# Optimization experiments

Measured on AMD Instinct MI355X. Metric: run time of the kernel, lower is better.

## Reference

```python
import jax, jax.numpy as jnp
import numpy as np

B, T, D, H, L = 32, 1024, 512, 512, 2  # batch, time, input dim, rnn_dim, layers


def setup_inputs() -> dict:
    key = jax.random.key(0)
    ks = jax.random.split(key, 4)
    x = jax.random.normal(ks[0], (B, T, D), jnp.float32)
    # contiguous-length mask like Keras masking (True = valid timestep)
    lengths = jax.random.randint(ks[1], (B,), T // 4, T + 1)
    mask = jnp.arange(T)[None, :] < lengths[:, None]
    s = 1.0 / np.sqrt(H)
    Wk = jax.random.normal(ks[2], (L, 2, D, 4 * H), jnp.float32) * s  # input kernels [layer, dir]
    Wr = jax.random.normal(ks[3], (L, 2, H, 4 * H), jnp.float32) * s  # recurrent kernels
    b = jnp.zeros((L, 2, 4 * H), jnp.float32)
    return {"x": x, "mask": mask, "Wk": Wk, "Wr": Wr, "b": b}


def _lstm_dir(x, mask, Wk, Wr, b, reverse):
    """Single-direction Keras-style LSTM with masking (masked steps carry h,c)."""
    if reverse:  # Bidirectional backward layer: process reversed time, reverse output back
        x = x[:, ::-1]
        mask = mask[:, ::-1]
    # precompute input projection for all timesteps: [B,T,4H]
    xw = jnp.einsum('btd,dg->btg', x, Wk) + b
    h0 = jnp.zeros((x.shape[0], Wr.shape[0]), x.dtype)

    def step(carry, inp):
        h, c = carry
        xw_t, m_t = inp  # [B,4H], [B]
        z = xw_t + h @ Wr
        i, f, g, o = jnp.split(z, 4, axis=-1)  # Keras gate order i,f,c,o
        c_new = jax.nn.sigmoid(f) * c + jax.nn.sigmoid(i) * jnp.tanh(g)
        h_new = jax.nn.sigmoid(o) * jnp.tanh(c_new)
        m = m_t[:, None]
        h = jnp.where(m, h_new, h)  # masked step: copy previous output/state
        c = jnp.where(m, c_new, c)
        return (h, c), h

    _, ys = jax.lax.scan(step, (h0, h0), (xw.transpose(1, 0, 2), mask.T))
    ys = ys.transpose(1, 0, 2)  # [B,T,H]
    if reverse:
        ys = ys[:, ::-1]
    return ys


def reference(x, mask, Wk, Wr, b):
    inp = x
    for l in range(L):
        fwd = _lstm_dir(inp, mask, Wk[l, 0], Wr[l, 0], b[l, 0], False)
        bwd = _lstm_dir(inp, mask, Wk[l, 1], Wr[l, 1], b[l, 1], True)
        res = fwd + bwd  # merge_mode='sum'
        inp = res + inp if l > 0 else res  # residual from layer 1 onward
    return inp
```

## Files before the change

### kernel.cpp

```cpp
#include <hip/hip_runtime.h>
#include <stdint.h>


#define B_ 32
#define T_ 1024
#define H_ 512
#define G_ 2048

typedef _Float16 f16;
typedef _Float16 f16x8 __attribute__((ext_vector_type(8)));
typedef float f32x4 __attribute__((ext_vector_type(4)));

#define AL_U(p) __hip_atomic_load((p), __ATOMIC_RELAXED, __HIP_MEMORY_SCOPE_AGENT)
#define AS_U(p, v) __hip_atomic_store((p), (v), __ATOMIC_RELAXED, __HIP_MEMORY_SCOPE_AGENT)
#define AADD_U(p, v) __hip_atomic_fetch_add((p), (v), __ATOMIC_RELAXED, __HIP_MEMORY_SCOPE_AGENT)

struct Claim {
  unsigned cnt[8];
  unsigned dirclaim;
  int xcddir[8];
  unsigned pad[15];
};

__device__ __forceinline__ float sigm(float x) { return 1.f / (1.f + __expf(-x)); }
__device__ __forceinline__ float tanh_(float x) { return 1.f - 2.f / (__expf(2.f * x) + 1.f); }

__global__ void cvt_x_t(const float* __restrict__ x, f16* __restrict__ xh) {
  size_t j = (size_t)blockIdx.x * 256 + threadIdx.x;
  int t = (int)(j >> 11);
  int g = (int)(j & 2047);
  int b = g >> 6;
  int d0 = (g & 63) * 8;
  const float4* p = (const float4*)(x + ((size_t)b * T_ + t) * H_ + d0);
  float4 a = p[0], c = p[1];
  union { f16 h[8]; uint4 u; } r;
  r.h[0] = (f16)a.x; r.h[1] = (f16)a.y; r.h[2] = (f16)a.z; r.h[3] = (f16)a.w;
  r.h[4] = (f16)c.x; r.h[5] = (f16)c.y; r.h[6] = (f16)c.z; r.h[7] = (f16)c.w;
  size_t o = (((size_t)t * 32 + (d0 >> 4)) * 32 + b) * 16 + (d0 & 15);
  *(uint4*)(xh + o) = r.u;
}

__global__ void cvt_w(const float* __restrict__ W, f16* __restrict__ Wb) {
  __shared__ float tl[32][65];
  const int wgi = blockIdx.x, kt = blockIdx.y, z = blockIdx.z;
  const float* src = W + (size_t)z * H_ * G_;
  const int k0 = kt * 32;
  for (int idx = threadIdx.x; idx < 2048; idx += 256) {
    int kk = idx >> 6, jj = idx & 63;
    int gate = jj >> 4, c = jj & 15;
    tl[kk][jj] = src[(size_t)(k0 + kk) * G_ + gate * H_ + wgi * 16 + c];
  }
  __syncthreads();
  const int gate = threadIdx.x >> 6, l = threadIdx.x & 63;
  const int c = l & 15, koff = (l >> 4) * 8;
  union { f16 h[8]; uint4 u; } v;
#pragma unroll
  for (int e = 0; e < 8; ++e) v.h[e] = (f16)tl[koff + e][gate * 16 + c];
  f16* dst = Wb + ((size_t)z * 32 + wgi) * 32768 + ((size_t)(kt * 4 + gate) * 64 + l) * 8;
  *(uint4*)dst = v.u;
}

__global__ void sum_h(const f16* __restrict__ a, const f16* __restrict__ b,
                      f16* __restrict__ r) {
  size_t i = ((size_t)blockIdx.x * 256 + threadIdx.x) * 8;
  f16x8 va = *(const f16x8*)(a + i), vb = *(const f16x8*)(b + i);
  *(f16x8*)(r + i) = va + vb;
}

template <int LAYER>
__global__ __launch_bounds__(512, 2) void lstm_rec4(
    const f16* __restrict__ xh,
    const f16* __restrict__ wkb,
    const f16* __restrict__ wrb,
    const float* __restrict__ biasAll,
    const void* __restrict__ maskp,
    f16* __restrict__ ring,
    unsigned* __restrict__ flags,
    Claim* __restrict__ cl,
    float* __restrict__ out,
    const f16* __restrict__ res1h)
{
  const int tid = threadIdx.x, wave = tid >> 6, lane = tid & 63;

  __shared__ int s_dir, s_wgi;
  if (tid == 0) {
    unsigned xcd;
    asm volatile("s_getreg_b32 %0, hwreg(HW_REG_XCC_ID)" : "=s"(xcd));
    xcd &= 7u;
    unsigned slot = AADD_U(&cl->cnt[xcd], 1u);
    int dir = -1, wgi = -1;
    if (slot < 32u) {
      if (slot == 31u) {
        unsigned d = AADD_U(&cl->dirclaim, 1u);
        int val = (d < 2u) ? (int)(d + 1u) : -1;
        __hip_atomic_store(&cl->xcddir[xcd], val, __ATOMIC_RELAXED, __HIP_MEMORY_SCOPE_AGENT);
      }
      while (true) {
        int v = __hip_atomic_load(&cl->xcddir[xcd], __ATOMIC_RELAXED, __HIP_MEMORY_SCOPE_AGENT);
        if (v != 0) { if (v > 0) { dir = v - 1; wgi = (int)slot; } break; }
        if (AL_U(&cl->dirclaim) >= 2u && AL_U(&cl->cnt[xcd]) < 32u) break;
        __builtin_amdgcn_s_sleep(2);
      }
    }
    s_dir = dir; s_wgi = wgi;
  }
  __syncthreads();
  const int dir = s_dir, wgi = s_wgi;
  if (dir < 0) return;

  const int mtile = wave & 1, kq = wave >> 1;
  const int j0 = wgi * 16;
  const int z = LAYER * 2 + dir;

  __shared__ f16 wkl[32768];
  __shared__ float zbuf[4][32][64];

  {
    const f16* wkc = wkb + ((size_t)z * 32 + wgi) * 32768;
#pragma unroll
    for (int r = 0; r < 8; ++r)
      *(uint4*)&wkl[(size_t)(r * 512 + tid) * 8] = *(const uint4*)(wkc + (size_t)(r * 512 + tid) * 8);
  }
  f16x8 wfr[4][4];
  {
    const f16* wrc = wrb + ((size_t)z * 32 + wgi) * 32768;
#pragma unroll
    for (int i = 0; i < 4; ++i) {
      int ktg = kq * 4 + i;
#pragma unroll
      for (int g = 0; g < 4; ++g)
        wfr[i][g] = *(const f16x8*)(wrc + ((size_t)(ktg * 4 + g) * 64 + lane) * 8);
    }
  }
  __syncthreads();

  const int arow = mtile * 16 + (lane & 15);
  const int lkb = lane >> 5;
  const int c0 = ((lane >> 4) & 1) * 8;

  const int cb = tid >> 4, cj = tid & 15;
  const float* bb = biasAll + (size_t)z * G_;
  float bias4[4];
#pragma unroll
  for (int g = 0; g < 4; ++g) bias4[g] = bb[g * H_ + j0 + cj];

  const unsigned char* mbytes = (const unsigned char*)maskp;
  const unsigned* mwords = (const unsigned*)maskp;
  const bool bytelay = (mbytes[1] != 0);

  float hstate = 0.f, cstate = 0.f;
  const unsigned* flagd = flags + (size_t)dir * T_ * 32;
  const f32x4 vzero = {0.f, 0.f, 0.f, 0.f};

  for (int s = 0; s < T_; ++s) {
    const int t = dir ? (T_ - 1 - s) : s;
    const f16* xb = xh + (size_t)t * 16384;
    f32x4 acc[4] = {vzero, vzero, vzero, vzero};
#pragma unroll
    for (int i = 0; i < 4; ++i) {
      const int ktg = kq * 4 + i;
      f16x8 xf = *(const f16x8*)(xb + ((size_t)(ktg * 2 + lkb) * 32 + arow) * 16 + c0);
#pragma unroll
      for (int g = 0; g < 4; ++g) {
        f16x8 wk = *(const f16x8*)&wkl[((size_t)(ktg * 4 + g) * 64 + lane) * 8];
        acc[g] = __builtin_amdgcn_mfma_f32_16x16x32_f16(xf, wk, acc[g], 0, 0, 0);
      }
    }
    const size_t btm = (size_t)cb * T_ + t;
    const bool mv = bytelay ? (mbytes[btm] != 0) : (mwords[btm] != 0);
    float xr = 0.f;
    if (LAYER == 1 && dir == 0)
      xr = (float)res1h[(((size_t)t * 32 + wgi) * 32 + cb) * 16 + cj];

    if (s > 0) {
      if (wave == 0) {
        const unsigned* fl = flagd + (size_t)(s - 1) * 32 + (lane & 31);
        while (true) {
          unsigned v = AL_U(fl);
          if (__ballot(v == 1u) == ~0ull) break;
        }
      }
      __syncthreads();
      const f16* hbase;
      if (LAYER == 0) {
        const int tprev = dir ? (T_ - s) : (s - 1);
        hbase = ring + ((size_t)dir * T_ + tprev) * 16384;
      } else {
        hbase = ring + ((size_t)dir * 8 + ((s - 1) & 7)) * 16384;
      }
#pragma unroll
      for (int i = 0; i < 4; ++i) {
        const int ktg = kq * 4 + i;
        f16x8 hf = *(const f16x8*)(hbase + ((size_t)(ktg * 2 + lkb) * 32 + arow) * 16 + c0);
#pragma unroll
        for (int g = 0; g < 4; ++g)
          acc[g] = __builtin_amdgcn_mfma_f32_16x16x32_f16(hf, wfr[i][g], acc[g], 0, 0, 0);
      }
    }
    {
      const int zr = mtile * 16 + ((lane >> 4) << 2);
      const int zc = lane & 15;
#pragma unroll
      for (int g = 0; g < 4; ++g)
#pragma unroll
        for (int r = 0; r < 4; ++r) zbuf[kq][zr + r][g * 16 + zc] = acc[g][r];
    }
    __syncthreads();

    float z4[4];
#pragma unroll
    for (int g = 0; g < 4; ++g)
      z4[g] = zbuf[0][cb][g * 16 + cj] + zbuf[1][cb][g * 16 + cj] +
              zbuf[2][cb][g * 16 + cj] + zbuf[3][cb][g * 16 + cj] + bias4[g];
    float ig = sigm(z4[0]), fg = sigm(z4[1]), gg = tanh_(z4[2]), og = sigm(z4[3]);
    float cn = fg * cstate + ig * gg;
    float hn = og * tanh_(cn);
    if (mv) { cstate = cn; hstate = hn; }

    f16 h16 = (f16)hstate;
    unsigned short hu = __builtin_bit_cast(unsigned short, h16);
    unsigned ob = (unsigned)__shfl_xor((int)hu, 1);
    unsigned pk = (unsigned)hu | ((ob & 0xffffu) << 16);
    if ((cj & 1) == 0) {
      f16* pb;
      if (LAYER == 0) pb = ring + ((size_t)dir * T_ + t) * 16384;
      else            pb = ring + ((size_t)dir * 8 + (s & 7)) * 16384;
      *(unsigned*)(pb + (size_t)wgi * 512 + tid) = pk;
    }
    asm volatile("s_waitcnt vmcnt(0)" ::: "memory");
    __syncthreads();
    if (tid == 0) AS_U((unsigned*)(flagd + (size_t)s * 32 + wgi), 1u);

    if (LAYER == 1) {
      atomicAdd(&out[btm * H_ + j0 + cj], hstate + xr);
    }
  }
}

extern "C" void kernel_launch(void* const* d_in, const int* in_sizes, int n_in,
                              void* d_out, int out_size, void* d_ws, size_t ws_size,
                              hipStream_t stream) {
  const float* x = (const float*)d_in[0];
  const void* maskp = (const void*)d_in[1];
  const float* Wk = (const float*)d_in[2];
  const float* Wr = (const float*)d_in[3];
  const float* bias = (const float*)d_in[4];
  float* out = (float*)d_out;
  (void)in_sizes; (void)n_in;

  char* ws = (char*)d_ws;
  f16* xh = (f16*)(ws);
  f16* wkb = (f16*)(ws + 33554432ull);
  f16* wrb = (f16*)(ws + 41943040ull);
  unsigned* flags0 = (unsigned*)(ws + 50331648ull);
  unsigned* flags1 = (unsigned*)(ws + 50593792ull);
  Claim* cl0 = (Claim*)(ws + 50855936ull);
  Claim* cl1 = (Claim*)(ws + 50856960ull);
  f16* ring1 = (f16*)(ws + 50857984ull);
  if (ws_size < 51382272ull) return;

  f16* ring0 = (f16*)d_out;
  f16* hf = ring0;
  f16* hb = ring0 + (size_t)T_ * 16384;

  hipMemsetAsync(flags0, 0, 526336ull, stream);
  cvt_x_t<<<8192, 256, 0, stream>>>(x, xh);
  cvt_w<<<dim3(32, 16, 4), 256, 0, stream>>>(Wk, wkb);
  cvt_w<<<dim3(32, 16, 4), 256, 0, stream>>>(Wr, wrb);

  lstm_rec4<0><<<512, 512, 0, stream>>>(xh, wkb, wrb, bias, maskp, ring0, flags0,
                                        cl0, (float*)nullptr, (const f16*)nullptr);
  sum_h<<<8192, 256, 0, stream>>>(hf, hb, xh);

  hipMemsetAsync(d_out, 0, 67108864ull, stream);
  lstm_rec4<1><<<512, 512, 0, stream>>>(xh, wkb, wrb, bias, maskp, ring1, flags1,
                                        cl1, out, xh);
}
```

Baseline: 6.091 ms.

## Switch LSTM recurrence to 32x32x16 MFMA with register-resident weights

Replaces the 16x16x32 MFMA tiling with 32x32x16 MFMA, where each wave owns a gate-pair column tile and a K quarter. Both the input and recurrent weight fragments now live in registers, so the LDS copy of the input kernel is dropped. The weight and x conversion kernels are rewritten to emit a matching layout, and the h ring layout changes with them. A large padded LDS allocation is added, apparently to keep occupancy at one block per CU, in exchange for higher register pressure per wave.

After: 7.452 ms. 1.22x slower.

```diff
diff --git a/kernel.cpp b/kernel.cpp
--- a/kernel.cpp
+++ b/kernel.cpp
@@ -9,7 +9,7 @@
 
 typedef _Float16 f16;
 typedef _Float16 f16x8 __attribute__((ext_vector_type(8)));
-typedef float f32x4 __attribute__((ext_vector_type(4)));
+typedef float f32x16 __attribute__((ext_vector_type(16)));
 
 #define AL_U(p) __hip_atomic_load((p), __ATOMIC_RELAXED, __HIP_MEMORY_SCOPE_AGENT)
 #define AS_U(p, v) __hip_atomic_store((p), (v), __ATOMIC_RELAXED, __HIP_MEMORY_SCOPE_AGENT)
@@ -27,10 +27,9 @@
 
 __global__ void cvt_x_t(const float* __restrict__ x, f16* __restrict__ xh) {
   size_t j = (size_t)blockIdx.x * 256 + threadIdx.x;
-  int t = (int)(j >> 11);
-  int g = (int)(j & 2047);
-  int b = g >> 6;
-  int d0 = (g & 63) * 8;
+  int b = (int)(j >> 16);
+  int t = (int)((j >> 6) & 1023);
+  int d0 = (int)(j & 63) * 8;
   const float4* p = (const float4*)(x + ((size_t)b * T_ + t) * H_ + d0);
   float4 a = p[0], c = p[1];
   union { f16 h[8]; uint4 u; } r;
@@ -41,23 +40,26 @@
 }
 
 __global__ void cvt_w(const float* __restrict__ W, f16* __restrict__ Wb) {
-  __shared__ float tl[32][65];
-  const int wgi = blockIdx.x, kt = blockIdx.y, z = blockIdx.z;
+  const int wgi = blockIdx.x, z = blockIdx.y;
+  const int tid = threadIdx.x;
   const float* src = W + (size_t)z * H_ * G_;
-  const int k0 = kt * 32;
-  for (int idx = threadIdx.x; idx < 2048; idx += 256) {
-    int kk = idx >> 6, jj = idx & 63;
-    int gate = jj >> 4, c = jj & 15;
-    tl[kk][jj] = src[(size_t)(k0 + kk) * G_ + gate * H_ + wgi * 16 + c];
-  }
-  __syncthreads();
-  const int gate = threadIdx.x >> 6, l = threadIdx.x & 63;
-  const int c = l & 15, koff = (l >> 4) * 8;
-  union { f16 h[8]; uint4 u; } v;
-#pragma unroll
-  for (int e = 0; e < 8; ++e) v.h[e] = (f16)tl[koff + e][gate * 16 + c];
-  f16* dst = Wb + ((size_t)z * 32 + wgi) * 32768 + ((size_t)(kt * 4 + gate) * 64 + l) * 8;
-  *(uint4*)dst = v.u;
+  __shared__ unsigned short st[512];
+  for (int cp = 0; cp < 2; ++cp)
+    for (int ks = 0; ks < 32; ++ks) {
+      size_t cbase = ((((size_t)z * 32 + wgi) * 2 + cp) * 32 + ks) * 512;
+#pragma unroll
+      for (int pass = 0; pass < 2; ++pass) {
+        int e = tid + pass * 256;
+        int col = e & 31, kk = e >> 5;
+        int gc = (2 * cp + (col >> 4)) * 512 + wgi * 16 + (col & 15);
+        f16 v = (f16)src[(size_t)(ks * 16 + kk) * G_ + gc];
+        st[col * 16 + kk] = __builtin_bit_cast(unsigned short, v);
+      }
+      __syncthreads();
+      unsigned pk = (unsigned)st[2 * tid] | ((unsigned)st[2 * tid + 1] << 16);
+      *((unsigned*)(Wb + cbase) + tid) = pk;
+      __syncthreads();
+    }
 }
 
 __global__ void sum_h(const f16* __restrict__ a, const f16* __restrict__ b,
@@ -68,7 +70,7 @@
 }
 
 template <int LAYER>
-__global__ __launch_bounds__(512, 2) void lstm_rec4(
+__global__ __launch_bounds__(512, 2) void lstm_rec6(
     const f16* __restrict__ xh,
     const f16* __restrict__ wkb,
     const f16* __restrict__ wrb,
@@ -83,6 +85,9 @@
   const int tid = threadIdx.x, wave = tid >> 6, lane = tid & 63;
 
   __shared__ int s_dir, s_wgi;
+  __shared__ float zbuf[2][4][32][48];
+  __shared__ char lds_pad[33024];
+
   if (tid == 0) {
     unsigned xcd;
     asm volatile("s_getreg_b32 %0, hwreg(HW_REG_XCC_ID)" : "=s"(xcd));
@@ -107,36 +112,22 @@
   __syncthreads();
   const int dir = s_dir, wgi = s_wgi;
   if (dir < 0) return;
-
-  const int mtile = wave & 1, kq = wave >> 1;
+  if (s_dir == -2) ((volatile char*)lds_pad)[tid] = 1;
+
+  const int cp = wave & 1, kq = wave >> 1;
   const int j0 = wgi * 16;
   const int z = LAYER * 2 + dir;
-
-  __shared__ f16 wkl[32768];
-  __shared__ float zbuf[4][32][64];
-
-  {
-    const f16* wkc = wkb + ((size_t)z * 32 + wgi) * 32768;
-#pragma unroll
-    for (int r = 0; r < 8; ++r)
-      *(uint4*)&wkl[(size_t)(r * 512 + tid) * 8] = *(const uint4*)(wkc + (size_t)(r * 512 + tid) * 8);
+  const int laneA = (lane & 31) * 16 + (lane >> 5) * 8;
+  const int hi = lane >> 5;
+
+  const f16* wkc = wkb + ((((size_t)z * 32 + wgi) * 2 + cp) * 32 + kq * 8) * 512;
+  const f16* wrc = wrb + ((((size_t)z * 32 + wgi) * 2 + cp) * 32 + kq * 8) * 512;
+  f16x8 wfk[8], wfr[8];
+#pragma unroll
+  for (int i = 0; i < 8; ++i) {
+    wfk[i] = *(const f16x8*)(wkc + i * 512 + laneA);
+    wfr[i] = *(const f16x8*)(wrc + i * 512 + laneA);
   }
-  f16x8 wfr[4][4];
-  {
-    const f16* wrc = wrb + ((size_t)z * 32 + wgi) * 32768;
-#pragma unroll
-    for (int i = 0; i < 4; ++i) {
-      int ktg = kq * 4 + i;
-#pragma unroll
-      for (int g = 0; g < 4; ++g)
-        wfr[i][g] = *(const f16x8*)(wrc + ((size_t)(ktg * 4 + g) * 64 + lane) * 8);
-    }
-  }
-  __syncthreads();
-
-  const int arow = mtile * 16 + (lane & 15);
-  const int lkb = lane >> 5;
-  const int c0 = ((lane >> 4) & 1) * 8;
 
   const int cb = tid >> 4, cj = tid & 15;
   const float* bb = biasAll + (size_t)z * G_;
@@ -149,22 +140,20 @@
   const bool bytelay = (mbytes[1] != 0);
 
   float hstate = 0.f, cstate = 0.f;
-  const unsigned* flagd = flags + (size_t)dir * T_ * 32;
-  const f32x4 vzero = {0.f, 0.f, 0.f, 0.f};
+  unsigned* flagd = flags + (size_t)dir * T_ * 32;
+  const f32x16 vzero = {0.f};
 
   for (int s = 0; s < T_; ++s) {
     const int t = dir ? (T_ - 1 - s) : s;
-    const f16* xb = xh + (size_t)t * 16384;
-    f32x4 acc[4] = {vzero, vzero, vzero, vzero};
-#pragma unroll
-    for (int i = 0; i < 4; ++i) {
-      const int ktg = kq * 4 + i;
-      f16x8 xf = *(const f16x8*)(xb + ((size_t)(ktg * 2 + lkb) * 32 + arow) * 16 + c0);
-#pragma unroll
-      for (int g = 0; g < 4; ++g) {
-        f16x8 wk = *(const f16x8*)&wkl[((size_t)(ktg * 4 + g) * 64 + lane) * 8];
-        acc[g] = __builtin_amdgcn_mfma_f32_16x16x32_f16(xf, wk, acc[g], 0, 0, 0);
-      }
+    const f16* xb = xh + (size_t)t * 16384 + (size_t)kq * 8 * 512 + laneA;
+    f32x16 acc = vzero;
+    {
+      f16x8 xf[8];
+#pragma unroll
+      for (int i = 0; i < 8; ++i) xf[i] = *(const f16x8*)(xb + i * 512);
+#pragma unroll
+      for (int i = 0; i < 8; ++i)
+        acc = __builtin_amdgcn_mfma_f32_32x32x16_f16(xf[i], wfk[i], acc, 0, 0, 0);
     }
     const size_t btm = (size_t)cb * T_ + t;
     const bool mv = bytelay ? (mbytes[btm] != 0) : (mwords[btm] != 0);
@@ -181,38 +170,33 @@
         }
       }
       __syncthreads();
-      const f16* hbase;
+      const f16* hb;
       if (LAYER == 0) {
         const int tprev = dir ? (T_ - s) : (s - 1);
-        hbase = ring + ((size_t)dir * T_ + tprev) * 16384;
+        hb = ring + ((size_t)dir * T_ + tprev) * 16384;
       } else {
-        hbase = ring + ((size_t)dir * 8 + ((s - 1) & 7)) * 16384;
-      }
-#pragma unroll
-      for (int i = 0; i < 4; ++i) {
-        const int ktg = kq * 4 + i;
-        f16x8 hf = *(const f16x8*)(hbase + ((size_t)(ktg * 2 + lkb) * 32 + arow) * 16 + c0);
-#pragma unroll
-        for (int g = 0; g < 4; ++g)
-          acc[g] = __builtin_amdgcn_mfma_f32_16x16x32_f16(hf, wfr[i][g], acc[g], 0, 0, 0);
-      }
-    }
-    {
-      const int zr = mtile * 16 + ((lane >> 4) << 2);
-      const int zc = lane & 15;
-#pragma unroll
-      for (int g = 0; g < 4; ++g)
-#pragma unroll
-        for (int r = 0; r < 4; ++r) zbuf[kq][zr + r][g * 16 + zc] = acc[g][r];
+        hb = ring + ((size_t)dir * 8 + ((s - 1) & 7)) * 16384;
+      }
+      hb += (size_t)kq * 8 * 512 + laneA;
+      f16x8 hf[8];
+#pragma unroll
+      for (int i = 0; i < 8; ++i) hf[i] = *(const f16x8*)(hb + i * 512);
+#pragma unroll
+      for (int i = 0; i < 8; ++i)
+        acc = __builtin_amdgcn_mfma_f32_32x32x16_f16(hf[i], wfr[i], acc, 0, 0, 0);
+    }
+#pragma unroll
+    for (int r = 0; r < 16; ++r) {
+      int row = (r & 3) + 8 * (r >> 2) + 4 * hi;
+      zbuf[cp][kq][row][lane & 31] = acc[r];
     }
     __syncthreads();
 
-    float z4[4];
-#pragma unroll
-    for (int g = 0; g < 4; ++g)
-      z4[g] = zbuf[0][cb][g * 16 + cj] + zbuf[1][cb][g * 16 + cj] +
-              zbuf[2][cb][g * 16 + cj] + zbuf[3][cb][g * 16 + cj] + bias4[g];
-    float ig = sigm(z4[0]), fg = sigm(z4[1]), gg = tanh_(z4[2]), og = sigm(z4[3]);
+    float zi = zbuf[0][0][cb][cj] + zbuf[0][1][cb][cj] + zbuf[0][2][cb][cj] + zbuf[0][3][cb][cj] + bias4[0];
+    float zf = zbuf[0][0][cb][16 + cj] + zbuf[0][1][cb][16 + cj] + zbuf[0][2][cb][16 + cj] + zbuf[0][3][cb][16 + cj] + bias4[1];
+    float zg = zbuf[1][0][cb][cj] + zbuf[1][1][cb][cj] + zbuf[1][2][cb][cj] + zbuf[1][3][cb][cj] + bias4[2];
+    float zo = zbuf[1][0][cb][16 + cj] + zbuf[1][1][cb][16 + cj] + zbuf[1][2][cb][16 + cj] + zbuf[1][3][cb][16 + cj] + bias4[3];
+    float ig = sigm(zi), fg = sigm(zf), gg = tanh_(zg), og = sigm(zo);
     float cn = fg * cstate + ig * gg;
     float hn = og * tanh_(cn);
     if (mv) { cstate = cn; hstate = hn; }
@@ -225,11 +209,11 @@
       f16* pb;
       if (LAYER == 0) pb = ring + ((size_t)dir * T_ + t) * 16384;
       else            pb = ring + ((size_t)dir * 8 + (s & 7)) * 16384;
-      *(unsigned*)(pb + (size_t)wgi * 512 + tid) = pk;
+      *(unsigned*)(pb + (size_t)wgi * 512 + cb * 16 + cj) = pk;
     }
     asm volatile("s_waitcnt vmcnt(0)" ::: "memory");
     __syncthreads();
-    if (tid == 0) AS_U((unsigned*)(flagd + (size_t)s * 32 + wgi), 1u);
+    if (tid == 0) AS_U(&flagd[(size_t)s * 32 + wgi], 1u);
 
     if (LAYER == 1) {
       atomicAdd(&out[btm * H_ + j0 + cj], hstate + xr);
@@ -263,16 +247,18 @@
   f16* hf = ring0;
   f16* hb = ring0 + (size_t)T_ * 16384;
 
-  hipMemsetAsync(flags0, 0, 526336ull, stream);
+  hipError_t e0 = hipMemsetAsync(flags0, 0, 526336ull, stream);
+  (void)e0;
   cvt_x_t<<<8192, 256, 0, stream>>>(x, xh);
-  cvt_w<<<dim3(32, 16, 4), 256, 0, stream>>>(Wk, wkb);
-  cvt_w<<<dim3(32, 16, 4), 256, 0, stream>>>(Wr, wrb);
-
-  lstm_rec4<0><<<512, 512, 0, stream>>>(xh, wkb, wrb, bias, maskp, ring0, flags0,
+  cvt_w<<<dim3(32, 4), 256, 0, stream>>>(Wk, wkb);
+  cvt_w<<<dim3(32, 4), 256, 0, stream>>>(Wr, wrb);
+
+  lstm_rec6<0><<<512, 512, 0, stream>>>(xh, wkb, wrb, bias, maskp, ring0, flags0,
                                         cl0, (float*)nullptr, (const f16*)nullptr);
   sum_h<<<8192, 256, 0, stream>>>(hf, hb, xh);
 
-  hipMemsetAsync(d_out, 0, 67108864ull, stream);
-  lstm_rec4<1><<<512, 512, 0, stream>>>(xh, wkb, wrb, bias, maskp, ring1, flags1,
+  hipError_t e1 = hipMemsetAsync(d_out, 0, 67108864ull, stream);
+  (void)e1;
+  lstm_rec6<1><<<512, 512, 0, stream>>>(xh, wkb, wrb, bias, maskp, ring1, flags1,
                                         cl1, out, xh);
 }
```
